# Kernel tuning notes

Measured on AMD Instinct MI355X. Metric: run time of the kernel, lower is better.

The kernel has to match this reference:

```python
import jax, jax.numpy as jnp
import numpy as np
import math

B, C, H, W = 32, 128, 32, 32
NUM_HEADS = 4
GROUPS = 32
EPS = 1e-5


def setup_inputs() -> dict:
    key = jax.random.key(0)
    ks = jax.random.split(key, 6)
    x = jax.random.normal(ks[0], (B, C, H, W), jnp.float32)
    norm_w = 1.0 + 0.1 * jax.random.normal(ks[1], (C,), jnp.float32)
    norm_b = 0.1 * jax.random.normal(ks[2], (C,), jnp.float32)
    qkv_w = jax.random.normal(ks[3], (3 * C, C), jnp.float32) / math.sqrt(C)
    proj_w = jax.random.normal(ks[4], (C, C), jnp.float32) / math.sqrt(C)
    proj_b = 0.01 * jax.random.normal(ks[5], (C,), jnp.float32)
    return {"x": x, "norm_w": norm_w, "norm_b": norm_b, "qkv_w": qkv_w,
            "proj_w": proj_w, "proj_b": proj_b}


def _group_norm(x, w, b):
    b_, c, h, w_ = x.shape
    xg = x.reshape(b_, GROUPS, c // GROUPS, h, w_)
    mu = xg.mean(axis=(2, 3, 4), keepdims=True)
    var = xg.var(axis=(2, 3, 4), keepdims=True)
    xn = ((xg - mu) * jax.lax.rsqrt(var + EPS)).reshape(b_, c, h, w_)
    return xn * w[None, :, None, None] + b[None, :, None, None]


def reference(x, norm_w, norm_b, qkv_w, proj_w, proj_b):
    b, c, h, w = x.shape
    nh = NUM_HEADS
    dh = c // nh
    hw = h * w
    xn = _group_norm(x, norm_w, norm_b)
    # 1x1 conv (no bias): [B,3C,H,W] flattened to [B,3C,HW]
    qkv = jnp.einsum('oc,bchw->bohw', qkv_w, xn).reshape(b, nh, 3 * dh, hw)
    # torch reshape (B*nh, 3C/nh, HW) + chunk(3, dim=1): per-head interleave
    q, k, v = qkv[:, :, :dh], qkv[:, :, dh:2 * dh], qkv[:, :, 2 * dh:]
    scale = 1.0 / math.sqrt(dh)
    # scale applied to BOTH q and k, as in the source
    attn = jnp.einsum('bhct,bhcs->bhts', q * scale, k * scale)  # [B,nh,HW,HW]
    attn = jax.nn.softmax(attn, axis=-1)
    hout = jnp.einsum('bhts,bhcs->bhct', attn, v).reshape(b, c, h, w)
    hout = jnp.einsum('oc,bchw->bohw', proj_w, hout) + proj_b[None, :, None, None]
    return hout + x
```

## Files before the change

### kernel.cpp

```cpp
#include <hip/hip_runtime.h>
#include <math.h>

#define BB 32
#define CC 128
#define HW 1024
#define NG 32
#define TPG 4096
#define QSZ ((size_t)BB * 4 * HW * 32)

typedef __attribute__((ext_vector_type(8))) short fragAB;
typedef __attribute__((ext_vector_type(4))) float fragC;

__device__ __forceinline__ ushort f2bf(float f) {
  union { float f; uint u; } v; v.f = f;
  uint r = v.u + 0x7FFFu + ((v.u >> 16) & 1u);
  return (ushort)(r >> 16);
}
__device__ __forceinline__ uint pack2(float lo, float hi) {
  return __builtin_amdgcn_perm(__float_as_uint(hi), __float_as_uint(lo), 0x07060302u);
}
__device__ __forceinline__ int vswz(int row, int g) {
  return row * 128 + 16 * (g ^ (row & 7));
}

__global__ __launch_bounds__(256) void gn_stats(const float* __restrict__ x,
    float2* __restrict__ stats, const float* __restrict__ qkvw,
    const float* __restrict__ projw, ushort* __restrict__ wq16,
    ushort* __restrict__ wp16) {
  if (blockIdx.x >= 1024) {
    int idx = (blockIdx.x - 1024) * 256 + threadIdx.x;
    if (idx < 49152) wq16[idx] = f2bf(qkvw[idx]);
    else             wp16[idx - 49152] = f2bf(projw[idx - 49152]);
    return;
  }
  int blk = blockIdx.x;
  int b = blk >> 5, g = blk & 31;
  const float4* xp4 = (const float4*)(x + ((size_t)(b * CC + g * 4)) * HW);
  float s = 0.f, s2 = 0.f;
  #pragma unroll
  for (int i = 0; i < 4; ++i) {
    float4 v = xp4[threadIdx.x + i * 256];
    s  += v.x + v.y + v.z + v.w;
    s2 += v.x * v.x + v.y * v.y + v.z * v.z + v.w * v.w;
  }
  #pragma unroll
  for (int off = 32; off; off >>= 1) {
    s  += __shfl_down(s, off, 64);
    s2 += __shfl_down(s2, off, 64);
  }
  __shared__ float ls[4], ls2[4];
  int lane = threadIdx.x & 63, wid = threadIdx.x >> 6;
  if (lane == 0) { ls[wid] = s; ls2[wid] = s2; }
  __syncthreads();
  if (threadIdx.x == 0) {
    float a  = ls[0] + ls[1] + ls[2] + ls[3];
    float a2 = ls2[0] + ls2[1] + ls2[2] + ls2[3];
    float mu = a * (1.f / TPG);
    float var = a2 * (1.f / TPG) - mu * mu;
    stats[blk] = make_float2(mu, rsqrtf(var + 1e-5f));
  }
}

__global__ __launch_bounds__(256) void gn_apply(const float* __restrict__ x,
    const float2* __restrict__ stats, const float* __restrict__ gw,
    const float* __restrict__ gb, ushort* __restrict__ xt16) {
  __shared__ ushort Xs[64][136];
  int b = blockIdx.x >> 4, t0 = (blockIdx.x & 15) * 64;
  int tid = threadIdx.x;
  int tq = tid & 15, cg = (tid >> 4) & 3, wv = tid >> 6;

  #pragma unroll
  for (int iter = 0; iter < 8; ++iter) {
    int c = wv * 4 + cg + iter * 16;
    float2 st = stats[b * 32 + (c >> 2)];
    float wsc = gw[c] * st.y;
    float bsc = gb[c] - st.x * wsc;
    const float* xp = x + ((size_t)b * CC + c) * HW + t0;
    #pragma unroll
    for (int j = 0; j < 4; ++j) {
      int t = tq + 16 * j;
      Xs[t][c] = f2bf(xp[t] * wsc + bsc);
    }
  }
  __syncthreads();
  #pragma unroll
  for (int it = 0; it < 4; ++it) {
    int row = (tid >> 4) + it * 16;
    int c8 = tid & 15;
    uint4 v = *(uint4*)&Xs[row][c8 * 8];
    *(uint4*)&xt16[((size_t)b * HW + t0 + row) * CC + c8 * 8] = v;
  }
}

template<int PROJ>
__global__ __launch_bounds__(256) void mgemm(
    const ushort* __restrict__ W16, const ushort* __restrict__ X16,
    ushort* __restrict__ Qb, float* __restrict__ out,
    const float* __restrict__ bias, const float* __restrict__ resid) {
  __shared__ ushort Xs[64 * 128];
  int b = blockIdx.z, o0 = blockIdx.y * 64, t0 = blockIdx.x * 64;
  int tid = threadIdx.x;
  int lane = tid & 63, w = tid >> 6, lc = lane & 15, lg = lane >> 4;
  int wo = w >> 1, wt = w & 1;

  fragAB af[2][4];
  #pragma unroll
  for (int i = 0; i < 2; ++i)
    #pragma unroll
    for (int kc = 0; kc < 4; ++kc)
      af[i][kc] = *(const fragAB*)&W16[(size_t)(o0 + wo * 32 + i * 16 + lc) * 128 + kc * 32 + lg * 8];

  {
    const char* src = (const char*)(X16 + ((size_t)b * HW + t0) * CC);
    char* dst = (char*)Xs;
    #pragma unroll
    for (int it = 0; it < 4; ++it) {
      int flat = tid * 16 + it * 4096;
      uint4 v = *(const uint4*)(src + flat);
      *(uint4*)(dst + (flat ^ (((flat >> 8) & 7) << 4))) = v;
    }
  }
  __syncthreads();

  fragC acc[2][2];
  #pragma unroll
  for (int i = 0; i < 2; ++i)
    #pragma unroll
    for (int j = 0; j < 2; ++j)
      acc[i][j] = (fragC){0.f, 0.f, 0.f, 0.f};

  #pragma unroll
  for (int kc = 0; kc < 4; ++kc) {
    fragAB bf[2];
    #pragma unroll
    for (int j = 0; j < 2; ++j) {
      int row = wt * 32 + j * 16 + lc;
      int byt = (row * 256 + kc * 64 + lg * 16) ^ ((row & 7) << 4);
      bf[j] = *(const fragAB*)((const char*)Xs + byt);
    }
    #pragma unroll
    for (int i = 0; i < 2; ++i)
      #pragma unroll
      for (int j = 0; j < 2; ++j)
        acc[i][j] = __builtin_amdgcn_mfma_f32_16x16x32_bf16(af[i][kc], bf[j], acc[i][j], 0, 0, 0);
  }

  if constexpr (PROJ == 0) {
    #pragma unroll
    for (int i = 0; i < 2; ++i) {
      int ob = o0 + wo * 32 + i * 16;
      int blk = ob >> 5;
      int hh = blk / 3, kind = blk % 3;
      size_t bh = (size_t)b * 4 + hh;
      float sc = (kind == 0) ? (0.03125f * 1.44269504f) : 1.f;
      #pragma unroll
      for (int j = 0; j < 2; ++j) {
        if (kind < 2) {
          ushort* dst = (kind == 0) ? Qb : (Qb + QSZ);
          int s16 = (t0 >> 4) + wt * 2 + j;
          int eo = s16 * 512 + (((ob & 16) >> 3) + (lg >> 1)) * 128 + lc * 8 + (lg & 1) * 4;
          ushort4 rv;
          rv.x = f2bf(acc[i][j][0] * sc); rv.y = f2bf(acc[i][j][1] * sc);
          rv.z = f2bf(acc[i][j][2] * sc); rv.w = f2bf(acc[i][j][3] * sc);
          *(ushort4*)&dst[bh * 32768 + eo] = rv;
        } else {
          ushort* Vb = Qb + 2 * QSZ;
          int eo = (t0 >> 6) * 2048 + ((ob & 16) >> 4) * 1024
                 + (wt * 4 + j * 2 + (lc >> 3)) * 128 + (lc & 7);
          #pragma unroll
          for (int r = 0; r < 4; ++r)
            Vb[bh * 32768 + eo + (lg * 4 + r) * 8] = f2bf(acc[i][j][r]);
        }
      }
    }
  } else {
    #pragma unroll
    for (int i = 0; i < 2; ++i)
      #pragma unroll
      for (int j = 0; j < 2; ++j) {
        int t = t0 + wt * 32 + j * 16 + lc;
        #pragma unroll
        for (int r = 0; r < 4; ++r) {
          int o = o0 + wo * 32 + i * 16 + lg * 4 + r;
          size_t idx = ((size_t)b * CC + o) * HW + t;
          out[idx] = acc[i][j][r] + bias[o] + resid[idx];
        }
      }
  }
}

__global__ __launch_bounds__(256) void attn5(
    const ushort* __restrict__ Qb, const ushort* __restrict__ Kb,
    const ushort* __restrict__ Vb, ushort* __restrict__ ao16) {
  __shared__ char arena[4][2560];

  int tid = threadIdx.x;
  int w = tid >> 6, lane = tid & 63, lc = lane & 15, lg = lane >> 4;
  int gw = (blockIdx.x & 7) * 512 + (blockIdx.x >> 3) * 4 + w;
  int bh = gw >> 5, tb = gw & 31;
  int h = bh & 3, b = bh >> 2;

  const ushort* Qg = Qb + (size_t)bh * 32768 + (size_t)(tb * 2) * 512 + lane * 8;
  const ushort* Kg = Kb + (size_t)bh * 32768 + lane * 8;
  const ushort* Vg = Vb + (size_t)bh * 32768 + lane * 8;
  int t0 = tb * 32;

  fragAB q0 = *(const fragAB*)&Qg[0];
  fragAB q1 = *(const fragAB*)&Qg[512];

  fragC a00 = {0.f,0.f,0.f,0.f}, a01 = {0.f,0.f,0.f,0.f};
  fragC a10 = {0.f,0.f,0.f,0.f}, a11 = {0.f,0.f,0.f,0.f};
  float l0 = 0.f, l1 = 0.f;
  char* PsB = arena[w];

  for (int i = 0; i < 16; ++i) {
    const ushort* Kt = Kg + i * 2048;
    const ushort* Vt = Vg + i * 2048;
    fragAB kf[4], vf[4];
    #pragma unroll
    for (int j = 0; j < 4; ++j) kf[j] = *(const fragAB*)&Kt[j * 512];
    #pragma unroll
    for (int u = 0; u < 4; ++u) vf[u] = *(const fragAB*)&Vt[u * 512];

    #pragma unroll
    for (int ts = 0; ts < 2; ++ts) {
      fragAB qf = ts ? q1 : q0;
      fragC S[4];
      #pragma unroll
      for (int j = 0; j < 4; ++j) {
        fragC z = {0.f,0.f,0.f,0.f};
        S[j] = __builtin_amdgcn_mfma_f32_16x16x32_bf16(kf[j], qf, z, 0, 0, 0);
      }
      float rs = 0.f;
      #pragma unroll
      for (int j = 0; j < 4; ++j) {
        float p0 = __builtin_amdgcn_exp2f(S[j][0]), p1 = __builtin_amdgcn_exp2f(S[j][1]);
        float p2 = __builtin_amdgcn_exp2f(S[j][2]), p3 = __builtin_amdgcn_exp2f(S[j][3]);
        rs += (p0 + p1) + (p2 + p3);
        uint2 wv2;
        wv2.x = pack2(p0, p1);
        wv2.y = pack2(p2, p3);
        int g = j * 2 + (lg >> 1);
        *(uint2*)(PsB + lc * 128 + 16 * (g ^ (lc & 7)) + (lg & 1) * 8) = wv2;
      }
      if (ts) l1 += rs; else l0 += rs;
      fragC* aA = ts ? &a01 : &a00;
      fragC* aB = ts ? &a11 : &a10;
      fragAB bp0 = *(const fragAB*)(PsB + vswz(lc, lg));
      fragAB bp1 = *(const fragAB*)(PsB + vswz(lc, 4 + lg));
      *aA = __builtin_amdgcn_mfma_f32_16x16x32_bf16(vf[0], bp0, *aA, 0, 0, 0);
      *aA = __builtin_amdgcn_mfma_f32_16x16x32_bf16(vf[1], bp1, *aA, 0, 0, 0);
      *aB = __builtin_amdgcn_mfma_f32_16x16x32_bf16(vf[2], bp0, *aB, 0, 0, 0);
      *aB = __builtin_amdgcn_mfma_f32_16x16x32_bf16(vf[3], bp1, *aB, 0, 0, 0);
    }
  }

  l0 += __shfl_xor(l0, 16); l0 += __shfl_xor(l0, 32);
  l1 += __shfl_xor(l1, 16); l1 += __shfl_xor(l1, 32);
  float il0 = 1.f / l0, il1 = 1.f / l1;

  ushort* Ol = (ushort*)arena[w];
  uint2 u;
  u.x = pack2(a00[0] * il0, a00[1] * il0); u.y = pack2(a00[2] * il0, a00[3] * il0);
  *(uint2*)&Ol[lc * 40 + lg * 4] = u;
  u.x = pack2(a10[0] * il0, a10[1] * il0); u.y = pack2(a10[2] * il0, a10[3] * il0);
  *(uint2*)&Ol[lc * 40 + 16 + lg * 4] = u;
  u.x = pack2(a01[0] * il1, a01[1] * il1); u.y = pack2(a01[2] * il1, a01[3] * il1);
  *(uint2*)&Ol[(lc + 16) * 40 + lg * 4] = u;
  u.x = pack2(a11[0] * il1, a11[1] * il1); u.y = pack2(a11[2] * il1, a11[3] * il1);
  *(uint2*)&Ol[(lc + 16) * 40 + 16 + lg * 4] = u;

  int row = lane >> 1, half = lane & 1;
  uint4 v0 = *(uint4*)&Ol[row * 40 + half * 16];
  uint4 v1 = *(uint4*)&Ol[row * 40 + half * 16 + 8];
  ushort* dst = &ao16[((size_t)b * HW + t0 + row) * CC + h * 32 + half * 16];
  *(uint4*)dst = v0;
  *(uint4*)(dst + 8) = v1;
}

extern "C" void kernel_launch(void* const* d_in, const int* in_sizes, int n_in,
                              void* d_out, int out_size, void* d_ws, size_t ws_size,
                              hipStream_t stream) {
  (void)in_sizes; (void)n_in; (void)out_size; (void)ws_size;
  const float* x     = (const float*)d_in[0];
  const float* gw    = (const float*)d_in[1];
  const float* gb    = (const float*)d_in[2];
  const float* qkvw  = (const float*)d_in[3];
  const float* projw = (const float*)d_in[4];
  const float* projb = (const float*)d_in[5];
  float* out = (float*)d_out;

  char* wsb = (char*)d_ws;
  ushort* xt16 = (ushort*)wsb;
  ushort* Qb   = (ushort*)(wsb + ((size_t)8 << 20));
  ushort* Kb   = Qb + QSZ;
  ushort* Vb   = Qb + 2 * QSZ;
  ushort* wq16 = (ushort*)(wsb + ((size_t)32 << 20));
  ushort* wp16 = (ushort*)(wsb + ((size_t)32 << 20) + (128 << 10));
  float2* stats = (float2*)(wsb + ((size_t)32 << 20) + (256 << 10));

  gn_stats<<<dim3(BB * NG + 256), 256, 0, stream>>>(x, stats, qkvw, projw, wq16, wp16);
  gn_apply<<<dim3(BB * 16), 256, 0, stream>>>(x, stats, gw, gb, xt16);
  mgemm<0><<<dim3(16, 6, BB), 256, 0, stream>>>(wq16, xt16, Qb, nullptr, nullptr, nullptr);
  attn5<<<dim3(1024), 256, 0, stream>>>(Qb, Kb, Vb, xt16);
  mgemm<1><<<dim3(16, 2, BB), 256, 0, stream>>>(wp16, xt16, nullptr, out, projb, x);
}
```

Before: 70.78 us.

## Fuse group-norm apply into QKV GEMM and split attention keys across waves

Removes the separate gn_apply kernel. The QKV GEMM now reads fp32 x directly, applies the group-norm scale and shift, and writes swizzled bf16 tiles into LDS. This saves one launch and the xt16 round trip through global memory, but each of the 6 output-channel blocks re-reads and re-normalizes the same x tile. Attention now splits the 16 key tiles between two waves per query tile, doubling the grid to 2048 blocks for more parallelism. The partial accumulators and row sums are merged through shared memory, at the cost of a block-wide sync and extra LDS.

```diff
diff --git a/kernel.cpp b/kernel.cpp
--- a/kernel.cpp
+++ b/kernel.cpp
@@ -10,6 +10,7 @@
 
 typedef __attribute__((ext_vector_type(8))) short fragAB;
 typedef __attribute__((ext_vector_type(4))) float fragC;
+typedef __attribute__((ext_vector_type(8))) ushort ushort8v;
 
 __device__ __forceinline__ ushort f2bf(float f) {
   union { float f; uint u; } v; v.f = f;
@@ -61,40 +62,11 @@
   }
 }
 
-__global__ __launch_bounds__(256) void gn_apply(const float* __restrict__ x,
-    const float2* __restrict__ stats, const float* __restrict__ gw,
-    const float* __restrict__ gb, ushort* __restrict__ xt16) {
-  __shared__ ushort Xs[64][136];
-  int b = blockIdx.x >> 4, t0 = (blockIdx.x & 15) * 64;
-  int tid = threadIdx.x;
-  int tq = tid & 15, cg = (tid >> 4) & 3, wv = tid >> 6;
-
-  #pragma unroll
-  for (int iter = 0; iter < 8; ++iter) {
-    int c = wv * 4 + cg + iter * 16;
-    float2 st = stats[b * 32 + (c >> 2)];
-    float wsc = gw[c] * st.y;
-    float bsc = gb[c] - st.x * wsc;
-    const float* xp = x + ((size_t)b * CC + c) * HW + t0;
-    #pragma unroll
-    for (int j = 0; j < 4; ++j) {
-      int t = tq + 16 * j;
-      Xs[t][c] = f2bf(xp[t] * wsc + bsc);
-    }
-  }
-  __syncthreads();
-  #pragma unroll
-  for (int it = 0; it < 4; ++it) {
-    int row = (tid >> 4) + it * 16;
-    int c8 = tid & 15;
-    uint4 v = *(uint4*)&Xs[row][c8 * 8];
-    *(uint4*)&xt16[((size_t)b * HW + t0 + row) * CC + c8 * 8] = v;
-  }
-}
-
 template<int PROJ>
 __global__ __launch_bounds__(256) void mgemm(
     const ushort* __restrict__ W16, const ushort* __restrict__ X16,
+    const float* __restrict__ xf, const float2* __restrict__ stats,
+    const float* __restrict__ gw, const float* __restrict__ gb,
     ushort* __restrict__ Qb, float* __restrict__ out,
     const float* __restrict__ bias, const float* __restrict__ resid) {
   __shared__ ushort Xs[64 * 128];
@@ -110,7 +82,37 @@
     for (int kc = 0; kc < 4; ++kc)
       af[i][kc] = *(const fragAB*)&W16[(size_t)(o0 + wo * 32 + i * 16 + lc) * 128 + kc * 32 + lg * 8];
 
-  {
+  if constexpr (PROJ == 0) {
+    int tq = tid & 15, co = tid >> 4;
+    const float* xb = xf + (size_t)b * CC * HW + t0 + tq * 4;
+    float wsc[8], bsc[8];
+    {
+      float2 s0 = stats[b * 32 + co * 2];
+      float2 s1 = stats[b * 32 + co * 2 + 1];
+      #pragma unroll
+      for (int cc = 0; cc < 8; ++cc) {
+        float rst = (cc < 4) ? s0.y : s1.y;
+        float mu  = (cc < 4) ? s0.x : s1.x;
+        float g = gw[co * 8 + cc];
+        wsc[cc] = g * rst;
+        bsc[cc] = gb[co * 8 + cc] - mu * wsc[cc];
+      }
+    }
+    union { float4 v; float f[4]; } vv[8];
+    #pragma unroll
+    for (int cc = 0; cc < 8; ++cc)
+      vv[cc].v = *(const float4*)&xb[(size_t)(co * 8 + cc) * HW];
+    #pragma unroll
+    for (int tt = 0; tt < 4; ++tt) {
+      int row = tq * 4 + tt;
+      ushort8v r;
+      #pragma unroll
+      for (int cc = 0; cc < 8; ++cc)
+        r[cc] = f2bf(vv[cc].f[tt] * wsc[cc] + bsc[cc]);
+      int byt = (row * 256 + co * 16) ^ ((row & 7) << 4);
+      *(ushort8v*)((char*)Xs + byt) = r;
+    }
+  } else {
     const char* src = (const char*)(X16 + ((size_t)b * HW + t0) * CC);
     char* dst = (char*)Xs;
     #pragma unroll
@@ -189,21 +191,24 @@
   }
 }
 
-__global__ __launch_bounds__(256) void attn5(
+__global__ __launch_bounds__(256) void attn6(
     const ushort* __restrict__ Qb, const ushort* __restrict__ Kb,
     const ushort* __restrict__ Vb, ushort* __restrict__ ao16) {
-  __shared__ char arena[4][2560];
+  __shared__ char arena[17408];
 
   int tid = threadIdx.x;
   int w = tid >> 6, lane = tid & 63, lc = lane & 15, lg = lane >> 4;
-  int gw = (blockIdx.x & 7) * 512 + (blockIdx.x >> 3) * 4 + w;
-  int bh = gw >> 5, tb = gw & 31;
+  int lb = blockIdx.x;
+  int gp = (lb & 7) * 256 + (lb >> 3);
+  int bh = gp >> 4, qp = gp & 15;
   int h = bh & 3, b = bh >> 2;
-
-  const ushort* Qg = Qb + (size_t)bh * 32768 + (size_t)(tb * 2) * 512 + lane * 8;
+  int qt = qp * 2 + (w >> 1);
+  int sh = w & 1;
+  int t0 = qt * 32;
+
+  const ushort* Qg = Qb + (size_t)bh * 32768 + (size_t)qt * 1024 + lane * 8;
   const ushort* Kg = Kb + (size_t)bh * 32768 + lane * 8;
   const ushort* Vg = Vb + (size_t)bh * 32768 + lane * 8;
-  int t0 = tb * 32;
 
   fragAB q0 = *(const fragAB*)&Qg[0];
   fragAB q1 = *(const fragAB*)&Qg[512];
@@ -211,9 +216,9 @@
   fragC a00 = {0.f,0.f,0.f,0.f}, a01 = {0.f,0.f,0.f,0.f};
   fragC a10 = {0.f,0.f,0.f,0.f}, a11 = {0.f,0.f,0.f,0.f};
   float l0 = 0.f, l1 = 0.f;
-  char* PsB = arena[w];
-
-  for (int i = 0; i < 16; ++i) {
+  char* PsB = arena + w * 2048;
+
+  for (int i = sh * 8; i < sh * 8 + 8; ++i) {
     const ushort* Kt = Kg + i * 2048;
     const ushort* Vt = Vg + i * 2048;
     fragAB kf[4], vf[4];
@@ -255,11 +260,37 @@
     }
   }
 
+  float* comb = (float*)(arena + 8192);
+  float* slot = comb + ((w >> 1) * 64 + lane) * 18;
+  if (sh == 1) {
+    #pragma unroll
+    for (int r = 0; r < 4; ++r) {
+      slot[r]      = a00[r];
+      slot[4 + r]  = a10[r];
+      slot[8 + r]  = a01[r];
+      slot[12 + r] = a11[r];
+    }
+    slot[16] = l0;
+    slot[17] = l1;
+  }
+  __syncthreads();
+  if (sh == 1) return;
+
+  #pragma unroll
+  for (int r = 0; r < 4; ++r) {
+    a00[r] += slot[r];
+    a10[r] += slot[4 + r];
+    a01[r] += slot[8 + r];
+    a11[r] += slot[12 + r];
+  }
+  l0 += slot[16];
+  l1 += slot[17];
+
   l0 += __shfl_xor(l0, 16); l0 += __shfl_xor(l0, 32);
   l1 += __shfl_xor(l1, 16); l1 += __shfl_xor(l1, 32);
   float il0 = 1.f / l0, il1 = 1.f / l1;
 
-  ushort* Ol = (ushort*)arena[w];
+  ushort* Ol = (ushort*)(arena + (w >> 1) * 4096);
   uint2 u;
   u.x = pack2(a00[0] * il0, a00[1] * il0); u.y = pack2(a00[2] * il0, a00[3] * il0);
   *(uint2*)&Ol[lc * 40 + lg * 4] = u;
@@ -291,7 +322,7 @@
   float* out = (float*)d_out;
 
   char* wsb = (char*)d_ws;
-  ushort* xt16 = (ushort*)wsb;
+  ushort* ao16 = (ushort*)wsb;
   ushort* Qb   = (ushort*)(wsb + ((size_t)8 << 20));
   ushort* Kb   = Qb + QSZ;
   ushort* Vb   = Qb + 2 * QSZ;
@@ -300,8 +331,9 @@
   float2* stats = (float2*)(wsb + ((size_t)32 << 20) + (256 << 10));
 
   gn_stats<<<dim3(BB * NG + 256), 256, 0, stream>>>(x, stats, qkvw, projw, wq16, wp16);
-  gn_apply<<<dim3(BB * 16), 256, 0, stream>>>(x, stats, gw, gb, xt16);
-  mgemm<0><<<dim3(16, 6, BB), 256, 0, stream>>>(wq16, xt16, Qb, nullptr, nullptr, nullptr);
-  attn5<<<dim3(1024), 256, 0, stream>>>(Qb, Kb, Vb, xt16);
-  mgemm<1><<<dim3(16, 2, BB), 256, 0, stream>>>(wp16, xt16, nullptr, out, projb, x);
-}
+  mgemm<0><<<dim3(16, 6, BB), 256, 0, stream>>>(wq16, nullptr, x, stats, gw, gb,
+                                                Qb, nullptr, nullptr, nullptr);
+  attn6<<<dim3(2048), 256, 0, stream>>>(Qb, Kb, Vb, ao16);
+  mgemm<1><<<dim3(16, 2, BB), 256, 0, stream>>>(wp16, ao16, nullptr, nullptr, nullptr, nullptr,
+                                                nullptr, out, projb, x);
+}
```

Measured after the change: 69.64 us. No clear change (-1.6%).
